# Optimization experiments

Hardware: AMD Instinct MI355X
Metric: run time of the kernel (lower is better)

## Reference

```python
import jax, jax.numpy as jnp
import numpy as np

B, H, S, D, E = 8, 12, 1024, 64, 8
NEG = 1000000.0  # mask penalty used by the original module

def setup_inputs() -> dict:
    key = jax.random.key(0)
    kq, kk, kv, kr, ki, km = jax.random.split(key, 6)
    Q = jax.random.normal(kq, (B, H, S, D), dtype=jnp.float32)
    K = jax.random.normal(kk, (B, H, S, D), dtype=jnp.float32)
    V = jax.random.normal(kv, (B, H, S, D), dtype=jnp.float32)
    route_mat = jax.random.uniform(kr, (B, E), dtype=jnp.float32)  # routing weights; grouping only
    ids = jax.random.randint(ki, (B,), 0, E, dtype=jnp.int64)       # expert id per sample
    mask = jax.random.randint(km, (B, S), 0, 2, dtype=jnp.int32)    # 1 = valid key position
    return {"Q": Q, "K": K, "V": V, "route_mat": route_mat, "ids": ids, "mask": mask}

def reference(Q, K, V, route_mat, ids, mask):
    # The torch module gathers batch samples per expert (ragged lists), runs
    # QK^T -> scale -> mask -> softmax -> (dropout p=0) -> @V per group, then
    # returns the grouped outputs. Grouping whole samples by expert is a pure
    # permutation of the batch, so the math equals per-sample attention; we
    # return results in the original batch order [B, H, S, D].
    scale = 1.0 / np.sqrt(D).astype(np.float32)
    maskf = mask.astype(Q.dtype)
    dot = jnp.einsum('bhqd,bhkd->bhqk', Q, K) * scale          # [B,H,S,S]
    dot = dot - NEG * (1.0 - maskf[:, None, None, :])
    attn = jax.nn.softmax(dot, axis=-1)
    return jnp.einsum('bhqk,bhkd->bhqd', attn, V)              # [B,H,S,D]
```

## Files before the change

kernel.cpp:

```cpp
#include <hip/hip_runtime.h>
#include <hip/hip_bf16.h>
#include <cstdint>
#include <cstddef>

#define HH 12
#define BH 96
#define SS 1024
#define DD 64
#define KT 64
#define QB 128
#define NQT (SS / QB)

typedef __attribute__((ext_vector_type(2))) float f32x2;
typedef __attribute__((ext_vector_type(4))) float f32x4;
typedef __attribute__((ext_vector_type(8))) short bf16x8;
typedef __attribute__((ext_vector_type(4))) int   i32x4;

#define SCL  0.1803368801111204f
#define NEGL 1442695.0f
#define THR  8.0f

__device__ __forceinline__ unsigned int pk2(float lo, float hi) {
    __hip_bfloat162 h = __float22bfloat162_rn(float2{lo, hi});
    unsigned int u;
    __builtin_memcpy(&u, &h, sizeof(u));
    return u;
}

__global__ __launch_bounds__(256) void prep_idx_kernel(
        const int* __restrict__ mask,
        int* __restrict__ idxbuf,
        int* __restrict__ nvalid) {
    __shared__ int sc[256];
    const int b   = blockIdx.x;
    const int tid = threadIdx.x;
    i32x4 m = *(const i32x4*)(mask + b * SS + tid * 4);
    int keep[4];
    int c = 0;
#pragma unroll
    for (int j = 0; j < 4; ++j) { keep[j] = (m[j] != 0); c += keep[j]; }
    sc[tid] = c;
    __syncthreads();
    for (int off = 1; off < 256; off <<= 1) {
        int v = (tid >= off) ? sc[tid - off] : 0;
        __syncthreads();
        sc[tid] += v;
        __syncthreads();
    }
    const int total = sc[255];
    int pos = sc[tid] - c;
    int* dst = idxbuf + b * SS;
    if (total == 0) {
#pragma unroll
        for (int j = 0; j < 4; ++j) dst[tid * 4 + j] = tid * 4 + j;
        if (tid == 0) nvalid[b] = SS;
        return;
    }
#pragma unroll
    for (int j = 0; j < 4; ++j)
        if (keep[j]) dst[pos++] = tid * 4 + j;
    const int padded = (total + 63) & ~63;
    for (int s = total + tid; s < padded; s += 256) dst[s] = 0;
    if (tid == 0) nvalid[b] = total;
}

__global__ __launch_bounds__(256, 3) void attn_kernel(
        const float* __restrict__ Q,
        const float* __restrict__ Kb,
        const float* __restrict__ Vb,
        const int* __restrict__ idxbuf,
        const int* __restrict__ nvalid,
        float* __restrict__ Out) {
    __shared__ unsigned short Klds[KT * DD];
    __shared__ unsigned short Vlds[DD * KT];
    __shared__ int idxLds[SS];

    const int tid  = threadIdx.x;
    const int w    = tid >> 6;
    const int lane = tid & 63;
    const int g    = lane >> 4;
    const int l15  = lane & 15;
    const int swq  = (l15 & 7) << 3;

    const int bh = blockIdx.x;
    const int qt = blockIdx.y;
    const int b  = bh / HH;

    ((i32x4*)idxLds)[tid] = ((const i32x4*)(idxbuf + b * SS))[tid];
    const int nv  = nvalid[b];
    const int NTb = (nv + 63) >> 6;

    bf16x8 qa[2][2];
#pragma unroll
    for (int h = 0; h < 2; ++h) {
        const float* qp = Q + ((size_t)(bh * SS + qt * QB + h * 64 + w * 16 + l15)) * DD + 8 * g;
#pragma unroll
        for (int c = 0; c < 2; ++c) {
            f32x4 lo = *(const f32x4*)(qp + c * 32);
            f32x4 hi = *(const f32x4*)(qp + c * 32 + 4);
            union { bf16x8 v; unsigned int u[4]; } o;
            o.u[0] = pk2(lo[0] * SCL, lo[1] * SCL);
            o.u[1] = pk2(lo[2] * SCL, lo[3] * SCL);
            o.u[2] = pk2(hi[0] * SCL, hi[1] * SCL);
            o.u[3] = pk2(hi[2] * SCL, hi[3] * SCL);
            qa[h][c] = o.v;
        }
    }

    f32x4 kreg[2][2];
    f32x2 vreg[8];
    const int vd0 = (tid & 31) * 2;
    const int vk0 = (tid >> 5) * 8;
    auto load_tile_regs = [&](int t) {
#pragma unroll
        for (int i = 0; i < 2; ++i) {
            int c = tid + i * 256;
            int row = c >> 3, d0 = (c & 7) * 8;
            int krow = idxLds[t * KT + row];
            const float* kp = Kb + ((size_t)(bh * SS + krow)) * DD + d0;
            kreg[i][0] = *(const f32x4*)kp;
            kreg[i][1] = *(const f32x4*)(kp + 4);
        }
        {
            i32x4 vi0 = *(const i32x4*)&idxLds[t * KT + vk0];
            i32x4 vi1 = *(const i32x4*)&idxLds[t * KT + vk0 + 4];
            const float* vbase = Vb + (size_t)(bh * SS) * DD + vd0;
#pragma unroll
            for (int j = 0; j < 4; ++j) vreg[j]     = *(const f32x2*)(vbase + (size_t)vi0[j] * DD);
#pragma unroll
            for (int j = 0; j < 4; ++j) vreg[4 + j] = *(const f32x2*)(vbase + (size_t)vi1[j] * DD);
        }
    };
    auto write_tile_lds = [&]() {
#pragma unroll
        for (int i = 0; i < 2; ++i) {
            int c = tid + i * 256;
            int row = c >> 3, d0 = (c & 7) * 8;
            union { bf16x8 v; unsigned int u[4]; } kv;
            kv.u[0] = pk2(kreg[i][0][0], kreg[i][0][1]);
            kv.u[1] = pk2(kreg[i][0][2], kreg[i][0][3]);
            kv.u[2] = pk2(kreg[i][1][0], kreg[i][1][1]);
            kv.u[3] = pk2(kreg[i][1][2], kreg[i][1][3]);
            *(bf16x8*)&Klds[row * DD + (d0 ^ ((row & 7) << 3))] = kv.v;
        }
        {
            union { bf16x8 v; unsigned int u[4]; } v0, v1;
            v0.u[0] = pk2(vreg[0][0], vreg[1][0]);
            v0.u[1] = pk2(vreg[2][0], vreg[3][0]);
            v0.u[2] = pk2(vreg[4][0], vreg[5][0]);
            v0.u[3] = pk2(vreg[6][0], vreg[7][0]);
            v1.u[0] = pk2(vreg[0][1], vreg[1][1]);
            v1.u[1] = pk2(vreg[2][1], vreg[3][1]);
            v1.u[2] = pk2(vreg[4][1], vreg[5][1]);
            v1.u[3] = pk2(vreg[6][1], vreg[7][1]);
            *(bf16x8*)&Vlds[vd0 * KT + (vk0 ^ ((vd0 & 7) << 3))] = v0.v;
            *(bf16x8*)&Vlds[(vd0 + 1) * KT + (vk0 ^ (((vd0 + 1) & 7) << 3))] = v1.v;
        }
    };

    f32x4 Oacc0[4], Oacc1[4];
#pragma unroll
    for (int dt = 0; dt < 4; ++dt) {
        Oacc0[dt] = (f32x4){0.f, 0.f, 0.f, 0.f};
        Oacc1[dt] = (f32x4){0.f, 0.f, 0.f, 0.f};
    }
    float m0 = -3.0e38f, m1 = -3.0e38f, l0 = 0.f, l1 = 0.f;

    __syncthreads();
    load_tile_regs(0);

#define SOFTMAX_H(s, mr, lr, Oa, pk)                                          \
    do {                                                                      \
        float tmax;                                                           \
        {                                                                     \
            f32x4 mm = s[0];                                                  \
            _Pragma("unroll")                                                 \
            for (int n = 1; n < 4; ++n)                                       \
                _Pragma("unroll")                                             \
                for (int r = 0; r < 4; ++r) mm[r] = fmaxf(mm[r], s[n][r]);    \
            tmax = fmaxf(fmaxf(mm[0], mm[1]), fmaxf(mm[2], mm[3]));           \
        }                                                                     \
        tmax = fmaxf(tmax, __shfl_xor(tmax, 16));                             \
        tmax = fmaxf(tmax, __shfl_xor(tmax, 32));                             \
        if (!__all(tmax <= mr + THR)) {                                       \
            float mnew = fmaxf(mr, tmax);                                     \
            float corr = __builtin_amdgcn_exp2f(mr - mnew);                   \
            mr = mnew;                                                        \
            lr *= corr;                                                       \
            float cq[4];                                                      \
            _Pragma("unroll")                                                 \
            for (int r = 0; r < 4; ++r) cq[r] = __shfl(corr, 4 * g + r);      \
            _Pragma("unroll")                                                 \
            for (int dt = 0; dt < 4; ++dt)                                    \
                _Pragma("unroll")                                             \
                for (int r = 0; r < 4; ++r) Oa[dt][r] *= cq[r];               \
        }                                                                     \
        float tsum = 0.f;                                                     \
        _Pragma("unroll")                                                     \
        for (int n = 0; n < 4; ++n) {                                         \
            float p0 = __builtin_amdgcn_exp2f(s[n][0] - mr);                  \
            float p1 = __builtin_amdgcn_exp2f(s[n][1] - mr);                  \
            float p2 = __builtin_amdgcn_exp2f(s[n][2] - mr);                  \
            float p3 = __builtin_amdgcn_exp2f(s[n][3] - mr);                  \
            tsum += (p0 + p1) + (p2 + p3);                                    \
            pk[n][0] = pk2(p0, p1);                                           \
            pk[n][1] = pk2(p2, p3);                                           \
        }                                                                     \
        tsum += __shfl_xor(tsum, 16);                                         \
        tsum += __shfl_xor(tsum, 32);                                         \
        lr += tsum;                                                           \
    } while (0)

#define REBUILD_PA(pk, ks, pa)                                                \
    do {                                                                      \
        auto sw0 = __builtin_amdgcn_permlane32_swap(pk[2 * ks][0], pk[2 * ks + 1][0], false, false); \
        auto sw1 = __builtin_amdgcn_permlane32_swap(pk[2 * ks][1], pk[2 * ks + 1][1], false, false); \
        auto sp0 = __builtin_amdgcn_permlane16_swap(sw0[0], sw0[1], false, false); \
        auto sp1 = __builtin_amdgcn_permlane16_swap(sw1[0], sw1[1], false, false); \
        pa.u[0] = sp0[0];                                                     \
        pa.u[2] = sp0[1];                                                     \
        pa.u[1] = sp1[0];                                                     \
        pa.u[3] = sp1[1];                                                     \
    } while (0)

#define QKT_BOTH(MMSTMT)                                                      \
    __builtin_amdgcn_s_setprio(1);                                            \
    _Pragma("unroll")                                                         \
    for (int n = 0; n < 4; ++n) {                                             \
        f32x4 mm; MMSTMT;                                                     \
        bf16x8 kb0 = *(const bf16x8*)&Klds[(16 * n + l15) * DD + ((8 * g) ^ swq)]; \
        bf16x8 kb1 = *(const bf16x8*)&Klds[(16 * n + l15) * DD + ((32 + 8 * g) ^ swq)]; \
        f32x4 a0 = __builtin_amdgcn_mfma_f32_16x16x32_bf16(kb0, qa[0][0], mm, 0, 0, 0); \
        s40[n]   = __builtin_amdgcn_mfma_f32_16x16x32_bf16(kb1, qa[0][1], a0, 0, 0, 0); \
        f32x4 a1 = __builtin_amdgcn_mfma_f32_16x16x32_bf16(kb0, qa[1][0], mm, 0, 0, 0); \
        s41[n]   = __builtin_amdgcn_mfma_f32_16x16x32_bf16(kb1, qa[1][1], a1, 0, 0, 0); \
    }                                                                         \
    __builtin_amdgcn_s_setprio(0);

#define SM_PV_BOTH()                                                          \
    {                                                                         \
        unsigned int pk0[4][2], pk1[4][2];                                    \
        SOFTMAX_H(s40, m0, l0, Oacc0, pk0);                                   \
        SOFTMAX_H(s41, m1, l1, Oacc1, pk1);                                   \
        __builtin_amdgcn_s_setprio(1);                                        \
        _Pragma("unroll")                                                     \
        for (int ks = 0; ks < 2; ++ks) {                                      \
            union { bf16x8 v; unsigned int u[4]; } pa0, pa1;                  \
            REBUILD_PA(pk0, ks, pa0);                                         \
            REBUILD_PA(pk1, ks, pa1);                                         \
            _Pragma("unroll")                                                 \
            for (int dt = 0; dt < 4; ++dt) {                                  \
                bf16x8 vb = *(const bf16x8*)                                  \
                    &Vlds[(dt * 16 + l15) * KT + ((ks * 32 + 8 * g) ^ swq)];  \
                Oacc0[dt] = __builtin_amdgcn_mfma_f32_16x16x32_bf16(pa0.v, vb, Oacc0[dt], 0, 0, 0); \
                Oacc1[dt] = __builtin_amdgcn_mfma_f32_16x16x32_bf16(pa1.v, vb, Oacc1[dt], 0, 0, 0); \
            }                                                                 \
        }                                                                     \
        __builtin_amdgcn_s_setprio(0);                                        \
    }

    for (int t = 0; t < NTb - 1; ++t) {
        __syncthreads();
        write_tile_lds();
        __syncthreads();
        load_tile_regs(t + 1);

        f32x4 s40[4], s41[4];
        QKT_BOTH({ mm[0] = 0.0f; mm[1] = 0.0f; mm[2] = 0.0f; mm[3] = 0.0f; });
        SM_PV_BOTH();
    }

    {
        __syncthreads();
        write_tile_lds();
        __syncthreads();

        const int lastbase = (NTb - 1) * KT + 4 * g;
        f32x4 s40[4], s41[4];
        QKT_BOTH({
            int slot = lastbase + 16 * n;
            mm[0] = (slot + 0 < nv) ? 0.0f : -NEGL;
            mm[1] = (slot + 1 < nv) ? 0.0f : -NEGL;
            mm[2] = (slot + 2 < nv) ? 0.0f : -NEGL;
            mm[3] = (slot + 3 < nv) ? 0.0f : -NEGL;
        });
        SM_PV_BOTH();
    }

#pragma unroll
    for (int h = 0; h < 2; ++h) {
        float inv = 1.0f / (h ? l1 : l0);
        float invq[4];
#pragma unroll
        for (int r = 0; r < 4; ++r) invq[r] = __shfl(inv, 4 * g + r);
        const size_t rowbase = (size_t)(bh * SS + qt * QB + h * 64 + w * 16);
#pragma unroll
        for (int dt = 0; dt < 4; ++dt)
#pragma unroll
            for (int r = 0; r < 4; ++r)
                Out[(rowbase + 4 * g + r) * DD + dt * 16 + l15] =
                    (h ? Oacc1[dt][r] : Oacc0[dt][r]) * invq[r];
    }
}

extern "C" void kernel_launch(void* const* d_in, const int* in_sizes, int n_in,
                              void* d_out, int out_size, void* d_ws, size_t ws_size,
                              hipStream_t stream) {
    const float* Q   = (const float*)d_in[0];
    const float* K   = (const float*)d_in[1];
    const float* V   = (const float*)d_in[2];
    const int* mask  = (const int*)d_in[5];
    float* out       = (float*)d_out;

    int* idxbuf = (int*)d_ws;
    int* nvalid = idxbuf + 8 * SS;

    prep_idx_kernel<<<dim3(8), 256, 0, stream>>>(mask, idxbuf, nvalid);
    attn_kernel<<<dim3(BH, NQT), 256, 0, stream>>>(Q, K, V, idxbuf, nvalid, out);
}
```

Before: 42.32 us.

## Precompact K/V to bf16 in workspace and read directly in attention

Adds a prep kernel that gathers the valid key rows of K and V once per head, converts them to bf16, and writes K compacted and V transposed into the workspace. A new attention kernel then reads the MFMA operands straight from global memory with no LDS staging or block barriers, instead of every query-tile block re-gathering and converting the same K/V tiles. This adds a kernel launch and an extra round-trip of compacted data through global memory, and relies on cache hits for the unstaged loads. The old staged kernel remains as a fallback when the workspace is too small.

```diff
diff --git a/kernel.cpp b/kernel.cpp
--- a/kernel.cpp
+++ b/kernel.cpp
@@ -26,148 +26,6 @@
     __builtin_memcpy(&u, &h, sizeof(u));
     return u;
 }
-
-__global__ __launch_bounds__(256) void prep_idx_kernel(
-        const int* __restrict__ mask,
-        int* __restrict__ idxbuf,
-        int* __restrict__ nvalid) {
-    __shared__ int sc[256];
-    const int b   = blockIdx.x;
-    const int tid = threadIdx.x;
-    i32x4 m = *(const i32x4*)(mask + b * SS + tid * 4);
-    int keep[4];
-    int c = 0;
-#pragma unroll
-    for (int j = 0; j < 4; ++j) { keep[j] = (m[j] != 0); c += keep[j]; }
-    sc[tid] = c;
-    __syncthreads();
-    for (int off = 1; off < 256; off <<= 1) {
-        int v = (tid >= off) ? sc[tid - off] : 0;
-        __syncthreads();
-        sc[tid] += v;
-        __syncthreads();
-    }
-    const int total = sc[255];
-    int pos = sc[tid] - c;
-    int* dst = idxbuf + b * SS;
-    if (total == 0) {
-#pragma unroll
-        for (int j = 0; j < 4; ++j) dst[tid * 4 + j] = tid * 4 + j;
-        if (tid == 0) nvalid[b] = SS;
-        return;
-    }
-#pragma unroll
-    for (int j = 0; j < 4; ++j)
-        if (keep[j]) dst[pos++] = tid * 4 + j;
-    const int padded = (total + 63) & ~63;
-    for (int s = total + tid; s < padded; s += 256) dst[s] = 0;
-    if (tid == 0) nvalid[b] = total;
-}
-
-__global__ __launch_bounds__(256, 3) void attn_kernel(
-        const float* __restrict__ Q,
-        const float* __restrict__ Kb,
-        const float* __restrict__ Vb,
-        const int* __restrict__ idxbuf,
-        const int* __restrict__ nvalid,
-        float* __restrict__ Out) {
-    __shared__ unsigned short Klds[KT * DD];
-    __shared__ unsigned short Vlds[DD * KT];
-    __shared__ int idxLds[SS];
-
-    const int tid  = threadIdx.x;
-    const int w    = tid >> 6;
-    const int lane = tid & 63;
-    const int g    = lane >> 4;
-    const int l15  = lane & 15;
-    const int swq  = (l15 & 7) << 3;
-
-    const int bh = blockIdx.x;
-    const int qt = blockIdx.y;
-    const int b  = bh / HH;
-
-    ((i32x4*)idxLds)[tid] = ((const i32x4*)(idxbuf + b * SS))[tid];
-    const int nv  = nvalid[b];
-    const int NTb = (nv + 63) >> 6;
-
-    bf16x8 qa[2][2];
-#pragma unroll
-    for (int h = 0; h < 2; ++h) {
-        const float* qp = Q + ((size_t)(bh * SS + qt * QB + h * 64 + w * 16 + l15)) * DD + 8 * g;
-#pragma unroll
-        for (int c = 0; c < 2; ++c) {
-            f32x4 lo = *(const f32x4*)(qp + c * 32);
-            f32x4 hi = *(const f32x4*)(qp + c * 32 + 4);
-            union { bf16x8 v; unsigned int u[4]; } o;
-            o.u[0] = pk2(lo[0] * SCL, lo[1] * SCL);
-            o.u[1] = pk2(lo[2] * SCL, lo[3] * SCL);
-            o.u[2] = pk2(hi[0] * SCL, hi[1] * SCL);
-            o.u[3] = pk2(hi[2] * SCL, hi[3] * SCL);
-            qa[h][c] = o.v;
-        }
-    }
-
-    f32x4 kreg[2][2];
-    f32x2 vreg[8];
-    const int vd0 = (tid & 31) * 2;
-    const int vk0 = (tid >> 5) * 8;
-    auto load_tile_regs = [&](int t) {
-#pragma unroll
-        for (int i = 0; i < 2; ++i) {
-            int c = tid + i * 256;
-            int row = c >> 3, d0 = (c & 7) * 8;
-            int krow = idxLds[t * KT + row];
-            const float* kp = Kb + ((size_t)(bh * SS + krow)) * DD + d0;
-            kreg[i][0] = *(const f32x4*)kp;
-            kreg[i][1] = *(const f32x4*)(kp + 4);
-        }
-        {
-            i32x4 vi0 = *(const i32x4*)&idxLds[t * KT + vk0];
-            i32x4 vi1 = *(const i32x4*)&idxLds[t * KT + vk0 + 4];
-            const float* vbase = Vb + (size_t)(bh * SS) * DD + vd0;
-#pragma unroll
-            for (int j = 0; j < 4; ++j) vreg[j]     = *(const f32x2*)(vbase + (size_t)vi0[j] * DD);
-#pragma unroll
-            for (int j = 0; j < 4; ++j) vreg[4 + j] = *(const f32x2*)(vbase + (size_t)vi1[j] * DD);
-        }
-    };
-    auto write_tile_lds = [&]() {
-#pragma unroll
-        for (int i = 0; i < 2; ++i) {
-            int c = tid + i * 256;
-            int row = c >> 3, d0 = (c & 7) * 8;
-            union { bf16x8 v; unsigned int u[4]; } kv;
-            kv.u[0] = pk2(kreg[i][0][0], kreg[i][0][1]);
-            kv.u[1] = pk2(kreg[i][0][2], kreg[i][0][3]);
-            kv.u[2] = pk2(kreg[i][1][0], kreg[i][1][1]);
-            kv.u[3] = pk2(kreg[i][1][2], kreg[i][1][3]);
-            *(bf16x8*)&Klds[row * DD + (d0 ^ ((row & 7) << 3))] = kv.v;
-        }
-        {
-            union { bf16x8 v; unsigned int u[4]; } v0, v1;
-            v0.u[0] = pk2(vreg[0][0], vreg[1][0]);
-            v0.u[1] = pk2(vreg[2][0], vreg[3][0]);
-            v0.u[2] = pk2(vreg[4][0], vreg[5][0]);
-            v0.u[3] = pk2(vreg[6][0], vreg[7][0]);
-            v1.u[0] = pk2(vreg[0][1], vreg[1][1]);
-            v1.u[1] = pk2(vreg[2][1], vreg[3][1]);
-            v1.u[2] = pk2(vreg[4][1], vreg[5][1]);
-            v1.u[3] = pk2(vreg[6][1], vreg[7][1]);
-            *(bf16x8*)&Vlds[vd0 * KT + (vk0 ^ ((vd0 & 7) << 3))] = v0.v;
-            *(bf16x8*)&Vlds[(vd0 + 1) * KT + (vk0 ^ (((vd0 + 1) & 7) << 3))] = v1.v;
-        }
-    };
-
-    f32x4 Oacc0[4], Oacc1[4];
-#pragma unroll
-    for (int dt = 0; dt < 4; ++dt) {
-        Oacc0[dt] = (f32x4){0.f, 0.f, 0.f, 0.f};
-        Oacc1[dt] = (f32x4){0.f, 0.f, 0.f, 0.f};
-    }
-    float m0 = -3.0e38f, m1 = -3.0e38f, l0 = 0.f, l1 = 0.f;
-
-    __syncthreads();
-    load_tile_regs(0);
 
 #define SOFTMAX_H(s, mr, lr, Oa, pk)                                          \
     do {                                                                      \
@@ -223,13 +81,13 @@
         pa.u[3] = sp1[1];                                                     \
     } while (0)
 
-#define QKT_BOTH(MMSTMT)                                                      \
+#define QKT_BOTH(MMSTMT, KB0, KB1)                                            \
     __builtin_amdgcn_s_setprio(1);                                            \
     _Pragma("unroll")                                                         \
     for (int n = 0; n < 4; ++n) {                                             \
         f32x4 mm; MMSTMT;                                                     \
-        bf16x8 kb0 = *(const bf16x8*)&Klds[(16 * n + l15) * DD + ((8 * g) ^ swq)]; \
-        bf16x8 kb1 = *(const bf16x8*)&Klds[(16 * n + l15) * DD + ((32 + 8 * g) ^ swq)]; \
+        bf16x8 kb0 = KB0;                                                     \
+        bf16x8 kb1 = KB1;                                                     \
         f32x4 a0 = __builtin_amdgcn_mfma_f32_16x16x32_bf16(kb0, qa[0][0], mm, 0, 0, 0); \
         s40[n]   = __builtin_amdgcn_mfma_f32_16x16x32_bf16(kb1, qa[0][1], a0, 0, 0, 0); \
         f32x4 a1 = __builtin_amdgcn_mfma_f32_16x16x32_bf16(kb0, qa[1][0], mm, 0, 0, 0); \
@@ -237,7 +95,7 @@
     }                                                                         \
     __builtin_amdgcn_s_setprio(0);
 
-#define SM_PV_BOTH()                                                          \
+#define SM_PV_BOTH(VB)                                                        \
     {                                                                         \
         unsigned int pk0[4][2], pk1[4][2];                                    \
         SOFTMAX_H(s40, m0, l0, Oacc0, pk0);                                   \
@@ -250,8 +108,7 @@
             REBUILD_PA(pk1, ks, pa1);                                         \
             _Pragma("unroll")                                                 \
             for (int dt = 0; dt < 4; ++dt) {                                  \
-                bf16x8 vb = *(const bf16x8*)                                  \
-                    &Vlds[(dt * 16 + l15) * KT + ((ks * 32 + 8 * g) ^ swq)];  \
+                bf16x8 vb = VB;                                               \
                 Oacc0[dt] = __builtin_amdgcn_mfma_f32_16x16x32_bf16(pa0.v, vb, Oacc0[dt], 0, 0, 0); \
                 Oacc1[dt] = __builtin_amdgcn_mfma_f32_16x16x32_bf16(pa1.v, vb, Oacc1[dt], 0, 0, 0); \
             }                                                                 \
@@ -259,15 +116,310 @@
         __builtin_amdgcn_s_setprio(0);                                        \
     }
 
+__global__ __launch_bounds__(256) void prep_idx_kernel(
+        const int* __restrict__ mask,
+        int* __restrict__ idxbuf,
+        int* __restrict__ nvalid) {
+    __shared__ int sc[256];
+    const int b   = blockIdx.x;
+    const int tid = threadIdx.x;
+    i32x4 m = *(const i32x4*)(mask + b * SS + tid * 4);
+    int keep[4];
+    int c = 0;
+#pragma unroll
+    for (int j = 0; j < 4; ++j) { keep[j] = (m[j] != 0); c += keep[j]; }
+    sc[tid] = c;
+    __syncthreads();
+    for (int off = 1; off < 256; off <<= 1) {
+        int v = (tid >= off) ? sc[tid - off] : 0;
+        __syncthreads();
+        sc[tid] += v;
+        __syncthreads();
+    }
+    const int total = sc[255];
+    int pos = sc[tid] - c;
+    int* dst = idxbuf + b * SS;
+    if (total == 0) {
+#pragma unroll
+        for (int j = 0; j < 4; ++j) dst[tid * 4 + j] = tid * 4 + j;
+        if (tid == 0) nvalid[b] = SS;
+        return;
+    }
+#pragma unroll
+    for (int j = 0; j < 4; ++j)
+        if (keep[j]) dst[pos++] = tid * 4 + j;
+    const int padded = (total + 63) & ~63;
+    for (int s = total + tid; s < padded; s += 256) dst[s] = 0;
+    if (tid == 0) nvalid[b] = total;
+}
+
+__global__ __launch_bounds__(256) void prep_kv_kernel(
+        const float* __restrict__ Kb,
+        const float* __restrict__ Vb,
+        const int* __restrict__ idxbuf,
+        const int* __restrict__ nvalid,
+        unsigned short* __restrict__ Kc,
+        unsigned short* __restrict__ VcT) {
+    __shared__ unsigned short vt[64][72];
+    const int bh = blockIdx.x;
+    const int t  = blockIdx.y;
+    const int b  = bh / HH;
+    const int padded = (nvalid[b] + 63) & ~63;
+    if (t * KT >= padded) return;
+
+    const int tid = threadIdx.x;
+    const int r   = tid >> 2;
+    const int d0  = (tid & 3) * 16;
+    const int slot = t * KT + r;
+    const int krow = idxbuf[b * SS + slot];
+
+    {
+        const float* kp = Kb + ((size_t)(bh * SS + krow)) * DD + d0;
+        f32x4 x0 = *(const f32x4*)(kp + 0);
+        f32x4 x1 = *(const f32x4*)(kp + 4);
+        f32x4 x2 = *(const f32x4*)(kp + 8);
+        f32x4 x3 = *(const f32x4*)(kp + 12);
+        union { bf16x8 v; unsigned int u[4]; } o0, o1;
+        o0.u[0] = pk2(x0[0], x0[1]); o0.u[1] = pk2(x0[2], x0[3]);
+        o0.u[2] = pk2(x1[0], x1[1]); o0.u[3] = pk2(x1[2], x1[3]);
+        o1.u[0] = pk2(x2[0], x2[1]); o1.u[1] = pk2(x2[2], x2[3]);
+        o1.u[2] = pk2(x3[0], x3[1]); o1.u[3] = pk2(x3[2], x3[3]);
+        unsigned short* dst = Kc + ((size_t)(bh * SS + slot)) * DD + d0;
+        *(bf16x8*)(dst)     = o0.v;
+        *(bf16x8*)(dst + 8) = o1.v;
+    }
+    {
+        const float* vp = Vb + ((size_t)(bh * SS + krow)) * DD + d0;
+        f32x4 x0 = *(const f32x4*)(vp + 0);
+        f32x4 x1 = *(const f32x4*)(vp + 4);
+        f32x4 x2 = *(const f32x4*)(vp + 8);
+        f32x4 x3 = *(const f32x4*)(vp + 12);
+        union { bf16x8 v; unsigned int u[4]; } o0, o1;
+        o0.u[0] = pk2(x0[0], x0[1]); o0.u[1] = pk2(x0[2], x0[3]);
+        o0.u[2] = pk2(x1[0], x1[1]); o0.u[3] = pk2(x1[2], x1[3]);
+        o1.u[0] = pk2(x2[0], x2[1]); o1.u[1] = pk2(x2[2], x2[3]);
+        o1.u[2] = pk2(x3[0], x3[1]); o1.u[3] = pk2(x3[2], x3[3]);
+        *(bf16x8*)&vt[r][d0]     = o0.v;
+        *(bf16x8*)&vt[r][d0 + 8] = o1.v;
+    }
+    __syncthreads();
+    {
+        const int d  = tid >> 2;
+        const int k0 = (tid & 3) * 16;
+        bf16x8 a, bvec;
+#pragma unroll
+        for (int j = 0; j < 8; ++j) a[j]    = (short)vt[k0 + j][d];
+#pragma unroll
+        for (int j = 0; j < 8; ++j) bvec[j] = (short)vt[k0 + 8 + j][d];
+        unsigned short* dst = VcT + ((size_t)(bh * DD + d)) * SS + t * KT + k0;
+        *(bf16x8*)(dst)     = a;
+        *(bf16x8*)(dst + 8) = bvec;
+    }
+}
+
+__global__ __launch_bounds__(256, 3) void attn_direct_kernel(
+        const float* __restrict__ Q,
+        const unsigned short* __restrict__ Kc,
+        const unsigned short* __restrict__ VcT,
+        const int* __restrict__ nvalid,
+        float* __restrict__ Out) {
+    const int tid  = threadIdx.x;
+    const int w    = tid >> 6;
+    const int lane = tid & 63;
+    const int g    = lane >> 4;
+    const int l15  = lane & 15;
+
+    const int bh = blockIdx.x;
+    const int qt = blockIdx.y;
+    const int b  = bh / HH;
+
+    const int nv  = nvalid[b];
+    const int NTb = (nv + 63) >> 6;
+
+    bf16x8 qa[2][2];
+#pragma unroll
+    for (int h = 0; h < 2; ++h) {
+        const float* qp = Q + ((size_t)(bh * SS + qt * QB + h * 64 + w * 16 + l15)) * DD + 8 * g;
+#pragma unroll
+        for (int c = 0; c < 2; ++c) {
+            f32x4 lo = *(const f32x4*)(qp + c * 32);
+            f32x4 hi = *(const f32x4*)(qp + c * 32 + 4);
+            union { bf16x8 v; unsigned int u[4]; } o;
+            o.u[0] = pk2(lo[0] * SCL, lo[1] * SCL);
+            o.u[1] = pk2(lo[2] * SCL, lo[3] * SCL);
+            o.u[2] = pk2(hi[0] * SCL, hi[1] * SCL);
+            o.u[3] = pk2(hi[2] * SCL, hi[3] * SCL);
+            qa[h][c] = o.v;
+        }
+    }
+
+    const unsigned short* Kbase = Kc  + (size_t)bh * SS * DD;
+    const unsigned short* Vbase = VcT + (size_t)bh * DD * SS;
+
+    f32x4 Oacc0[4], Oacc1[4];
+#pragma unroll
+    for (int dt = 0; dt < 4; ++dt) {
+        Oacc0[dt] = (f32x4){0.f, 0.f, 0.f, 0.f};
+        Oacc1[dt] = (f32x4){0.f, 0.f, 0.f, 0.f};
+    }
+    float m0 = -3.0e38f, m1 = -3.0e38f, l0 = 0.f, l1 = 0.f;
+
     for (int t = 0; t < NTb - 1; ++t) {
+        f32x4 s40[4], s41[4];
+        QKT_BOTH({ mm[0] = 0.0f; mm[1] = 0.0f; mm[2] = 0.0f; mm[3] = 0.0f; },
+                 (*(const bf16x8*)(Kbase + (size_t)(t * KT + 16 * n + l15) * DD + 8 * g)),
+                 (*(const bf16x8*)(Kbase + (size_t)(t * KT + 16 * n + l15) * DD + 32 + 8 * g)));
+        SM_PV_BOTH((*(const bf16x8*)(Vbase + (size_t)(dt * 16 + l15) * SS + t * KT + ks * 32 + 8 * g)));
+    }
+
+    {
+        const int t = NTb - 1;
+        const int lastbase = t * KT + 4 * g;
+        f32x4 s40[4], s41[4];
+        QKT_BOTH({
+            int slot = lastbase + 16 * n;
+            mm[0] = (slot + 0 < nv) ? 0.0f : -NEGL;
+            mm[1] = (slot + 1 < nv) ? 0.0f : -NEGL;
+            mm[2] = (slot + 2 < nv) ? 0.0f : -NEGL;
+            mm[3] = (slot + 3 < nv) ? 0.0f : -NEGL;
+        },
+                 (*(const bf16x8*)(Kbase + (size_t)(t * KT + 16 * n + l15) * DD + 8 * g)),
+                 (*(const bf16x8*)(Kbase + (size_t)(t * KT + 16 * n + l15) * DD + 32 + 8 * g)));
+        SM_PV_BOTH((*(const bf16x8*)(Vbase + (size_t)(dt * 16 + l15) * SS + t * KT + ks * 32 + 8 * g)));
+    }
+
+#pragma unroll
+    for (int h = 0; h < 2; ++h) {
+        float inv = 1.0f / (h ? l1 : l0);
+        float invq[4];
+#pragma unroll
+        for (int r = 0; r < 4; ++r) invq[r] = __shfl(inv, 4 * g + r);
+        const size_t rowbase = (size_t)(bh * SS + qt * QB + h * 64 + w * 16);
+#pragma unroll
+        for (int dt = 0; dt < 4; ++dt)
+#pragma unroll
+            for (int r = 0; r < 4; ++r)
+                Out[(rowbase + 4 * g + r) * DD + dt * 16 + l15] =
+                    (h ? Oacc1[dt][r] : Oacc0[dt][r]) * invq[r];
+    }
+}
+
+__global__ __launch_bounds__(256, 3) void attn_staged_kernel(
+        const float* __restrict__ Q,
+        const float* __restrict__ Kb,
+        const float* __restrict__ Vb,
+        const int* __restrict__ idxbuf,
+        const int* __restrict__ nvalid,
+        float* __restrict__ Out) {
+    __shared__ unsigned short Klds[KT * DD];
+    __shared__ unsigned short Vlds[DD * KT];
+    __shared__ int idxLds[SS];
+
+    const int tid  = threadIdx.x;
+    const int w    = tid >> 6;
+    const int lane = tid & 63;
+    const int g    = lane >> 4;
+    const int l15  = lane & 15;
+    const int swq  = (l15 & 7) << 3;
+
+    const int bh = blockIdx.x;
+    const int qt = blockIdx.y;
+    const int b  = bh / HH;
+
+    ((i32x4*)idxLds)[tid] = ((const i32x4*)(idxbuf + b * SS))[tid];
+    const int nv  = nvalid[b];
+    const int NTb = (nv + 63) >> 6;
+
+    bf16x8 qa[2][2];
+#pragma unroll
+    for (int h = 0; h < 2; ++h) {
+        const float* qp = Q + ((size_t)(bh * SS + qt * QB + h * 64 + w * 16 + l15)) * DD + 8 * g;
+#pragma unroll
+        for (int c = 0; c < 2; ++c) {
+            f32x4 lo = *(const f32x4*)(qp + c * 32);
+            f32x4 hi = *(const f32x4*)(qp + c * 32 + 4);
+            union { bf16x8 v; unsigned int u[4]; } o;
+            o.u[0] = pk2(lo[0] * SCL, lo[1] * SCL);
+            o.u[1] = pk2(lo[2] * SCL, lo[3] * SCL);
+            o.u[2] = pk2(hi[0] * SCL, hi[1] * SCL);
+            o.u[3] = pk2(hi[2] * SCL, hi[3] * SCL);
+            qa[h][c] = o.v;
+        }
+    }
+
+    f32x4 kreg[2][2];
+    f32x2 vreg[8];
+    const int vd0 = (tid & 31) * 2;
+    const int vk0 = (tid >> 5) * 8;
+    auto load_tile_regs = [&](int t) {
+#pragma unroll
+        for (int i = 0; i < 2; ++i) {
+            int c = tid + i * 256;
+            int row = c >> 3, d0 = (c & 7) * 8;
+            int krow = idxLds[t * KT + row];
+            const float* kp = Kb + ((size_t)(bh * SS + krow)) * DD + d0;
+            kreg[i][0] = *(const f32x4*)kp;
+            kreg[i][1] = *(const f32x4*)(kp + 4);
+        }
+        {
+            i32x4 vi0 = *(const i32x4*)&idxLds[t * KT + vk0];
+            i32x4 vi1 = *(const i32x4*)&idxLds[t * KT + vk0 + 4];
+            const float* vbase = Vb + (size_t)(bh * SS) * DD + vd0;
+#pragma unroll
+            for (int j = 0; j < 4; ++j) vreg[j]     = *(const f32x2*)(vbase + (size_t)vi0[j] * DD);
+#pragma unroll
+            for (int j = 0; j < 4; ++j) vreg[4 + j] = *(const f32x2*)(vbase + (size_t)vi1[j] * DD);
+        }
+    };
+    auto write_tile_lds = [&]() {
+#pragma unroll
+        for (int i = 0; i < 2; ++i) {
+            int c = tid + i * 256;
+            int row = c >> 3, d0 = (c & 7) * 8;
+            union { bf16x8 v; unsigned int u[4]; } kv;
+            kv.u[0] = pk2(kreg[i][0][0], kreg[i][0][1]);
+            kv.u[1] = pk2(kreg[i][0][2], kreg[i][0][3]);
+            kv.u[2] = pk2(kreg[i][1][0], kreg[i][1][1]);
+            kv.u[3] = pk2(kreg[i][1][2], kreg[i][1][3]);
+            *(bf16x8*)&Klds[row * DD + (d0 ^ ((row & 7) << 3))] = kv.v;
+        }
+        {
+            union { bf16x8 v; unsigned int u[4]; } v0, v1;
+            v0.u[0] = pk2(vreg[0][0], vreg[1][0]);
+            v0.u[1] = pk2(vreg[2][0], vreg[3][0]);
+            v0.u[2] = pk2(vreg[4][0], vreg[5][0]);
+            v0.u[3] = pk2(vreg[6][0], vreg[7][0]);
+            v1.u[0] = pk2(vreg[0][1], vreg[1][1]);
+            v1.u[1] = pk2(vreg[2][1], vreg[3][1]);
+            v1.u[2] = pk2(vreg[4][1], vreg[5][1]);
+            v1.u[3] = pk2(vreg[6][1], vreg[7][1]);
+            *(bf16x8*)&Vlds[vd0 * KT + (vk0 ^ ((vd0 & 7) << 3))] = v0.v;
+            *(bf16x8*)&Vlds[(vd0 + 1) * KT + (vk0 ^ (((vd0 + 1) & 7) << 3))] = v1.v;
+        }
+    };
+
+    f32x4 Oacc0[4], Oacc1[4];
+#pragma unroll
+    for (int dt = 0; dt < 4; ++dt) {
+        Oacc0[dt] = (f32x4){0.f, 0.f, 0.f, 0.f};
+        Oacc1[dt] = (f32x4){0.f, 0.f, 0.f, 0.f};
+    }
+    float m0 = -3.0e38f, m1 = -3.0e38f, l0 = 0.f, l1 = 0.f;
+
+    __syncthreads();
+    load_tile_regs(0);
+
+    for (int t = 0; t < NTb - 1; ++t) {
         __syncthreads();
         write_tile_lds();
         __syncthreads();
         load_tile_regs(t + 1);
 
         f32x4 s40[4], s41[4];
-        QKT_BOTH({ mm[0] = 0.0f; mm[1] = 0.0f; mm[2] = 0.0f; mm[3] = 0.0f; });
-        SM_PV_BOTH();
+        QKT_BOTH({ mm[0] = 0.0f; mm[1] = 0.0f; mm[2] = 0.0f; mm[3] = 0.0f; },
+                 (*(const bf16x8*)&Klds[(16 * n + l15) * DD + ((8 * g) ^ swq)]),
+                 (*(const bf16x8*)&Klds[(16 * n + l15) * DD + ((32 + 8 * g) ^ swq)]));
+        SM_PV_BOTH((*(const bf16x8*)&Vlds[(dt * 16 + l15) * KT + ((ks * 32 + 8 * g) ^ swq)]));
     }
 
     {
@@ -283,8 +435,10 @@
             mm[1] = (slot + 1 < nv) ? 0.0f : -NEGL;
             mm[2] = (slot + 2 < nv) ? 0.0f : -NEGL;
             mm[3] = (slot + 3 < nv) ? 0.0f : -NEGL;
-        });
-        SM_PV_BOTH();
+        },
+                 (*(const bf16x8*)&Klds[(16 * n + l15) * DD + ((8 * g) ^ swq)]),
+                 (*(const bf16x8*)&Klds[(16 * n + l15) * DD + ((32 + 8 * g) ^ swq)]));
+        SM_PV_BOTH((*(const bf16x8*)&Vlds[(dt * 16 + l15) * KT + ((ks * 32 + 8 * g) ^ swq)]));
     }
 
 #pragma unroll
@@ -315,6 +469,17 @@
     int* idxbuf = (int*)d_ws;
     int* nvalid = idxbuf + 8 * SS;
 
+    const size_t kc_elems = (size_t)BH * SS * DD;
+    const size_t need = 8 * SS * 4 + 64 + 2 * kc_elems * 2;
+
     prep_idx_kernel<<<dim3(8), 256, 0, stream>>>(mask, idxbuf, nvalid);
-    attn_kernel<<<dim3(BH, NQT), 256, 0, stream>>>(Q, K, V, idxbuf, nvalid, out);
-}
+
+    if (ws_size >= need) {
+        unsigned short* Kc  = (unsigned short*)(nvalid + 16);
+        unsigned short* VcT = Kc + kc_elems;
+        prep_kv_kernel<<<dim3(BH, SS / KT), 256, 0, stream>>>(K, V, idxbuf, nvalid, Kc, VcT);
+        attn_direct_kernel<<<dim3(BH, NQT), 256, 0, stream>>>(Q, Kc, VcT, nvalid, out);
+    } else {
+        attn_staged_kernel<<<dim3(BH, NQT), 256, 0, stream>>>(Q, K, V, idxbuf, nvalid, out);
+    }
+}
```

New measurement: 69.99 us. +65.4%, slower.

## Halve query tile to 64 rows per block, one query group per wave

Applied to the files above, without the earlier changes.

Shrinks the per-block query tile from 128 to 64 rows, so each wave processes one 16-row query group instead of two, and raises the launch-bounds occupancy hint from 3 to 4. This doubles the grid size and lowers register pressure, which allows more waves per CU and better latency hiding. In exchange, each K/V tile loaded and converted into LDS is reused by half as many query rows, so global K/V traffic and bf16 conversion work per output double.

```diff
diff --git a/kernel.cpp b/kernel.cpp
--- a/kernel.cpp
+++ b/kernel.cpp
@@ -8,7 +8,7 @@
 #define SS 1024
 #define DD 64
 #define KT 64
-#define QB 128
+#define QB 64
 #define NQT (SS / QB)
 
 typedef __attribute__((ext_vector_type(2))) float f32x2;
@@ -64,7 +64,7 @@
     if (tid == 0) nvalid[b] = total;
 }
 
-__global__ __launch_bounds__(256, 3) void attn_kernel(
+__global__ __launch_bounds__(256, 4) void attn_kernel(
         const float* __restrict__ Q,
         const float* __restrict__ Kb,
         const float* __restrict__ Vb,
@@ -90,10 +90,9 @@
     const int nv  = nvalid[b];
     const int NTb = (nv + 63) >> 6;
 
-    bf16x8 qa[2][2];
-#pragma unroll
-    for (int h = 0; h < 2; ++h) {
-        const float* qp = Q + ((size_t)(bh * SS + qt * QB + h * 64 + w * 16 + l15)) * DD + 8 * g;
+    bf16x8 qa[2];
+    {
+        const float* qp = Q + ((size_t)(bh * SS + qt * QB + w * 16 + l15)) * DD + 8 * g;
 #pragma unroll
         for (int c = 0; c < 2; ++c) {
             f32x4 lo = *(const f32x4*)(qp + c * 32);
@@ -103,7 +102,7 @@
             o.u[1] = pk2(lo[2] * SCL, lo[3] * SCL);
             o.u[2] = pk2(hi[0] * SCL, hi[1] * SCL);
             o.u[3] = pk2(hi[2] * SCL, hi[3] * SCL);
-            qa[h][c] = o.v;
+            qa[c] = o.v;
         }
     }
 
@@ -158,13 +157,10 @@
         }
     };
 
-    f32x4 Oacc0[4], Oacc1[4];
-#pragma unroll
-    for (int dt = 0; dt < 4; ++dt) {
-        Oacc0[dt] = (f32x4){0.f, 0.f, 0.f, 0.f};
-        Oacc1[dt] = (f32x4){0.f, 0.f, 0.f, 0.f};
-    }
-    float m0 = -3.0e38f, m1 = -3.0e38f, l0 = 0.f, l1 = 0.f;
+    f32x4 Oacc0[4];
+#pragma unroll
+    for (int dt = 0; dt < 4; ++dt) Oacc0[dt] = (f32x4){0.f, 0.f, 0.f, 0.f};
+    float m0 = -3.0e38f, l0 = 0.f;
 
     __syncthreads();
     load_tile_regs(0);
@@ -223,37 +219,32 @@
         pa.u[3] = sp1[1];                                                     \
     } while (0)
 
-#define QKT_BOTH(MMSTMT)                                                      \
+#define QKT_ONE(MMSTMT)                                                       \
     __builtin_amdgcn_s_setprio(1);                                            \
     _Pragma("unroll")                                                         \
     for (int n = 0; n < 4; ++n) {                                             \
         f32x4 mm; MMSTMT;                                                     \
         bf16x8 kb0 = *(const bf16x8*)&Klds[(16 * n + l15) * DD + ((8 * g) ^ swq)]; \
         bf16x8 kb1 = *(const bf16x8*)&Klds[(16 * n + l15) * DD + ((32 + 8 * g) ^ swq)]; \
-        f32x4 a0 = __builtin_amdgcn_mfma_f32_16x16x32_bf16(kb0, qa[0][0], mm, 0, 0, 0); \
-        s40[n]   = __builtin_amdgcn_mfma_f32_16x16x32_bf16(kb1, qa[0][1], a0, 0, 0, 0); \
-        f32x4 a1 = __builtin_amdgcn_mfma_f32_16x16x32_bf16(kb0, qa[1][0], mm, 0, 0, 0); \
-        s41[n]   = __builtin_amdgcn_mfma_f32_16x16x32_bf16(kb1, qa[1][1], a1, 0, 0, 0); \
+        f32x4 a0 = __builtin_amdgcn_mfma_f32_16x16x32_bf16(kb0, qa[0], mm, 0, 0, 0); \
+        s40[n]   = __builtin_amdgcn_mfma_f32_16x16x32_bf16(kb1, qa[1], a0, 0, 0, 0); \
     }                                                                         \
     __builtin_amdgcn_s_setprio(0);
 
-#define SM_PV_BOTH()                                                          \
+#define SM_PV_ONE()                                                           \
     {                                                                         \
-        unsigned int pk0[4][2], pk1[4][2];                                    \
+        unsigned int pk0[4][2];                                               \
         SOFTMAX_H(s40, m0, l0, Oacc0, pk0);                                   \
-        SOFTMAX_H(s41, m1, l1, Oacc1, pk1);                                   \
         __builtin_amdgcn_s_setprio(1);                                        \
         _Pragma("unroll")                                                     \
         for (int ks = 0; ks < 2; ++ks) {                                      \
-            union { bf16x8 v; unsigned int u[4]; } pa0, pa1;                  \
+            union { bf16x8 v; unsigned int u[4]; } pa0;                       \
             REBUILD_PA(pk0, ks, pa0);                                         \
-            REBUILD_PA(pk1, ks, pa1);                                         \
             _Pragma("unroll")                                                 \
             for (int dt = 0; dt < 4; ++dt) {                                  \
                 bf16x8 vb = *(const bf16x8*)                                  \
                     &Vlds[(dt * 16 + l15) * KT + ((ks * 32 + 8 * g) ^ swq)];  \
                 Oacc0[dt] = __builtin_amdgcn_mfma_f32_16x16x32_bf16(pa0.v, vb, Oacc0[dt], 0, 0, 0); \
-                Oacc1[dt] = __builtin_amdgcn_mfma_f32_16x16x32_bf16(pa1.v, vb, Oacc1[dt], 0, 0, 0); \
             }                                                                 \
         }                                                                     \
         __builtin_amdgcn_s_setprio(0);                                        \
@@ -265,9 +256,9 @@
         __syncthreads();
         load_tile_regs(t + 1);
 
-        f32x4 s40[4], s41[4];
-        QKT_BOTH({ mm[0] = 0.0f; mm[1] = 0.0f; mm[2] = 0.0f; mm[3] = 0.0f; });
-        SM_PV_BOTH();
+        f32x4 s40[4];
+        QKT_ONE({ mm[0] = 0.0f; mm[1] = 0.0f; mm[2] = 0.0f; mm[3] = 0.0f; });
+        SM_PV_ONE();
     }
 
     {
@@ -276,30 +267,28 @@
         __syncthreads();
 
         const int lastbase = (NTb - 1) * KT + 4 * g;
-        f32x4 s40[4], s41[4];
-        QKT_BOTH({
+        f32x4 s40[4];
+        QKT_ONE({
             int slot = lastbase + 16 * n;
             mm[0] = (slot + 0 < nv) ? 0.0f : -NEGL;
             mm[1] = (slot + 1 < nv) ? 0.0f : -NEGL;
             mm[2] = (slot + 2 < nv) ? 0.0f : -NEGL;
             mm[3] = (slot + 3 < nv) ? 0.0f : -NEGL;
         });
-        SM_PV_BOTH();
-    }
-
-#pragma unroll
-    for (int h = 0; h < 2; ++h) {
-        float inv = 1.0f / (h ? l1 : l0);
+        SM_PV_ONE();
+    }
+
+    {
+        float inv = 1.0f / l0;
         float invq[4];
 #pragma unroll
         for (int r = 0; r < 4; ++r) invq[r] = __shfl(inv, 4 * g + r);
-        const size_t rowbase = (size_t)(bh * SS + qt * QB + h * 64 + w * 16);
+        const size_t rowbase = (size_t)(bh * SS + qt * QB + w * 16);
 #pragma unroll
         for (int dt = 0; dt < 4; ++dt)
 #pragma unroll
             for (int r = 0; r < 4; ++r)
-                Out[(rowbase + 4 * g + r) * DD + dt * 16 + l15] =
-                    (h ? Oacc1[dt][r] : Oacc0[dt][r]) * invq[r];
+                Out[(rowbase + 4 * g + r) * DD + dt * 16 + l15] = Oacc0[dt][r] * invq[r];
     }
 }
 
```

Result: slower. 47.89 us (+13.2%).
